# Performance work log

Measured on AMD Instinct MI355X. Metric: run time of the kernel, lower is better.

Reference implementation:

```python
import jax, jax.numpy as jnp
import numpy as np

D_MODEL = 1024
N_HEADS = 16
HEAD_DIM = D_MODEL // N_HEADS
SEQ_LEN = 2048
BATCH = 2
THETA = 10000.0


def _rope_tables(dim, seq_len, theta=THETA):
    freqs = 1.0 / theta ** (jnp.arange(0, dim, 2, dtype=jnp.float32) / dim)  # (dim/2,)
    t = jnp.arange(seq_len, dtype=jnp.float32)
    ang = jnp.outer(t, freqs)  # (S, dim/2)
    # interleave each freq twice to match the (-x_odd, x_even) rotation layout
    cos = jnp.repeat(jnp.cos(ang), 2, axis=-1)  # (S, dim)
    sin = jnp.repeat(jnp.sin(ang), 2, axis=-1)
    return cos, sin


def _apply_rope(x, cos, sin):
    # x: (B, S, H, D); cos/sin: (S, D)
    x_rot = jnp.stack([-x[..., 1::2], x[..., ::2]], axis=-1).reshape(x.shape)
    return x * cos[None, :, None, :] + x_rot * sin[None, :, None, :]


def setup_inputs() -> dict:
    key = jax.random.key(0)
    ks = jax.random.split(key, 9)
    s = 1.0 / np.sqrt(D_MODEL)
    return {
        "x": jax.random.normal(ks[0], (BATCH, SEQ_LEN, D_MODEL), dtype=jnp.float32),
        "wq": jax.random.normal(ks[1], (D_MODEL, D_MODEL), jnp.float32) * s,
        "bq": jnp.zeros((D_MODEL,), jnp.float32),
        "wk": jax.random.normal(ks[2], (D_MODEL, D_MODEL), jnp.float32) * s,
        "bk": jnp.zeros((D_MODEL,), jnp.float32),
        "wv": jax.random.normal(ks[3], (D_MODEL, D_MODEL), jnp.float32) * s,
        "bv": jnp.zeros((D_MODEL,), jnp.float32),
        "wo": jax.random.normal(ks[4], (D_MODEL, D_MODEL), jnp.float32) * s,
        "bo": jnp.zeros((D_MODEL,), jnp.float32),
    }


def reference(x, wq, bq, wk, bk, wv, bv, wo, bo):
    B, S, _ = x.shape
    cos, sin = _rope_tables(HEAD_DIM, S)
    # projections (torch Linear: x @ W^T + b)
    q = (x @ wq.T + bq).reshape(B, S, N_HEADS, HEAD_DIM)
    k = (x @ wk.T + bk).reshape(B, S, N_HEADS, HEAD_DIM)
    v = (x @ wv.T + bv).reshape(B, S, N_HEADS, HEAD_DIM)
    q = _apply_rope(q, cos, sin)
    k = _apply_rope(k, cos, sin)
    # attention: bhqd, bhkd -> bhqk
    scale = 1.0 / np.sqrt(HEAD_DIM)
    scores = jnp.einsum("bqhd,bkhd->bhqk", q, k) * scale
    attn = jax.nn.softmax(scores, axis=-1)
    out = jnp.einsum("bhqk,bkhd->bqhd", attn, v).reshape(B, S, D_MODEL)
    return out @ wo.T + bo
```

## Files before the change

### kernel.cpp

```cpp
#include <hip/hip_runtime.h>

typedef __attribute__((ext_vector_type(8))) __bf16 bf16x8;
typedef __attribute__((ext_vector_type(4))) __bf16 bf16x4;
typedef __attribute__((ext_vector_type(4))) float f32x4;
typedef __attribute__((ext_vector_type(4))) unsigned short ushort4v;

__device__ __forceinline__ unsigned short f2bf(float f) {
  unsigned u = __builtin_bit_cast(unsigned, f);
  u += 0x7fffu + ((u >> 16) & 1u);
  return (unsigned short)(u >> 16);
}

__device__ __forceinline__ void gload16(const void* g, void* l) {
  __builtin_amdgcn_global_load_lds(
      (const __attribute__((address_space(1))) void*)g,
      (__attribute__((address_space(3))) void*)l, 16, 0, 0);
}

__global__ __launch_bounds__(256) void convert_k(
    const float* __restrict__ x, const float* __restrict__ wq,
    const float* __restrict__ wk, const float* __restrict__ wv,
    const float* __restrict__ wo,
    unsigned short* __restrict__ xb, unsigned short* __restrict__ wqkv,
    unsigned short* __restrict__ wob, float* cosT, float* sinT) {
  if (blockIdx.x >= 8192) {
    const int idx = (blockIdx.x - 8192) * 256 + threadIdx.x;
    const int s = idx >> 5, j = idx & 31;
    const float freq = powf(10000.f, -(float)(2 * j) * (1.f / 64.f));
    const float ang = (float)s * freq;
    cosT[idx] = cosf(ang);
    sinT[idx] = sinf(ang);
    return;
  }
  const size_t i = ((size_t)blockIdx.x * 256 + threadIdx.x) * 4;
  const float* src; unsigned short* dst; size_t off;
  if (i < 4194304)      { src = x;  dst = xb;              off = i; }
  else if (i < 5242880) { src = wq; dst = wqkv;            off = i - 4194304; }
  else if (i < 6291456) { src = wk; dst = wqkv + 1048576;  off = i - 5242880; }
  else if (i < 7340032) { src = wv; dst = wqkv + 2097152;  off = i - 6291456; }
  else                  { src = wo; dst = wob;             off = i - 7340032; }
  f32x4 v = *(const f32x4*)(src + off);
  ushort4v o;
  o[0] = f2bf(v[0]); o[1] = f2bf(v[1]); o[2] = f2bf(v[2]); o[3] = f2bf(v[3]);
  *(ushort4v*)(dst + off) = o;
}

template <int EPI>
__global__ __launch_bounds__(256) void gemm_bt_k(
    const unsigned short* __restrict__ A, const unsigned short* __restrict__ B,
    int M, int N, int K,
    unsigned short* __restrict__ Qr, unsigned short* __restrict__ Kr,
    unsigned short* __restrict__ Vt,
    const float* __restrict__ bq, const float* __restrict__ bk,
    const float* __restrict__ bvv,
    const float* __restrict__ cosT, const float* __restrict__ sinT,
    float* __restrict__ Cout, const float* __restrict__ bias) {
  __shared__ char smem[32768];
  const int t = threadIdx.x;
  const int wave = t >> 6, lane = t & 63;
  const int l15 = lane & 15, g = lane >> 4;
  const int nt = N >> 7;
  const int mb = (blockIdx.x / nt) << 7;
  const int nb = (blockIdx.x % nt) << 7;
  const int wm = (wave >> 1) << 6;
  const int wn = (wave & 1) << 6;

  const f32x4 zv = {0.f, 0.f, 0.f, 0.f};
  f32x4 acc[4][4];
#pragma unroll
  for (int i = 0; i < 4; i++)
#pragma unroll
    for (int j = 0; j < 4; j++) acc[i][j] = zv;

  for (int kt = 0; kt < K; kt += 64) {
#pragma unroll
    for (int i = 0; i < 4; i++) {
      const int lin = t * 16 + i * 4096;
      const int r = lin >> 7;
      const int cb = (lin & 127) ^ ((r & 7) << 4);
      gload16((const char*)A + ((size_t)(mb + r) * K + kt) * 2 + cb,
              smem + i * 4096 + wave * 1024);
      gload16((const char*)B + ((size_t)(nb + r) * K + kt) * 2 + cb,
              smem + 16384 + i * 4096 + wave * 1024);
    }
    __syncthreads();

    bf16x8 af[4][2], bfr[4][2];
    const int sw = (l15 & 7) << 4;
#pragma unroll
    for (int mf = 0; mf < 4; mf++) {
      const int r = wm + mf * 16 + l15;
      const int r2 = wn + mf * 16 + l15;
#pragma unroll
      for (int kf = 0; kf < 2; kf++) {
        af[mf][kf]  = *(const bf16x8*)(smem + r * 128 + ((kf * 64 + g * 16) ^ sw));
        bfr[mf][kf] = *(const bf16x8*)(smem + 16384 + r2 * 128 + ((kf * 64 + g * 16) ^ sw));
      }
    }
#pragma unroll
    for (int mf = 0; mf < 4; mf++)
#pragma unroll
      for (int nf = 0; nf < 4; nf++) {
        acc[mf][nf] = __builtin_amdgcn_mfma_f32_16x16x32_bf16(af[mf][0], bfr[nf][0], acc[mf][nf], 0, 0, 0);
        acc[mf][nf] = __builtin_amdgcn_mfma_f32_16x16x32_bf16(af[mf][1], bfr[nf][1], acc[mf][nf], 0, 0, 0);
      }
    __syncthreads();
  }

#pragma unroll
  for (int mf = 0; mf < 4; mf++) {
#pragma unroll
    for (int nf = 0; nf < 4; nf++) {
      const int row0 = mb + wm + mf * 16 + g * 4;
      const int col = nb + wn + nf * 16 + l15;
      if (EPI == 1) {
        const float bsv = bias[col];
#pragma unroll
        for (int r = 0; r < 4; r++)
          Cout[(size_t)(row0 + r) * N + col] = acc[mf][nf][r] + bsv;
      } else {
        const int region = col >> 10;
        const int cc = col & 1023;
        const int h = cc >> 6, d = cc & 63;
        const float bias_v = (region == 0 ? bq : (region == 1 ? bk : bvv))[cc];
        if (region < 2) {
          unsigned short* Ob = (region == 0 ? Qr : Kr);
          const float scl = (region == 0) ? 0.180336880111120425f : 1.0f;
#pragma unroll
          for (int r = 0; r < 4; r++) {
            const int row = row0 + r;
            const int s = row & 2047;
            const int b = row >> 11;
            const float v = acc[mf][nf][r] + bias_v;
            const float p = __shfl_xor(v, 1);
            const float c = cosT[s * 32 + (d >> 1)];
            const float sn = sinT[s * 32 + (d >> 1)];
            float o = (d & 1) ? (v * c + p * sn) : (v * c - p * sn);
            o *= scl;
            Ob[((size_t)(b * 16 + h) * 2048 + s) * 64 + d] = f2bf(o);
          }
        } else {
          ushort4v w;
#pragma unroll
          for (int r = 0; r < 4; r++) w[r] = f2bf(acc[mf][nf][r] + bias_v);
          const int s = row0 & 2047;
          const int b = row0 >> 11;
          *(ushort4v*)(Vt + ((size_t)(b * 16 + h) * 64 + d) * 2048 + s) = w;
        }
      }
    }
  }
}

__global__ __launch_bounds__(256, 4) void flash_k(
    const unsigned short* __restrict__ Qr, const unsigned short* __restrict__ Kr,
    const unsigned short* __restrict__ Vt, unsigned short* __restrict__ Oa) {
  __shared__ char smem[40960];
  const int bid = blockIdx.x;
  const int bh = ((bid & 7) << 2) | ((bid >> 3) & 3);
  const int qt = bid >> 5;
  const int t = threadIdx.x;
  const int wave = t >> 6, lane = t & 63;
  const int l15 = lane & 15, g = lane >> 4;
  char* pbuf = smem + 32768 + wave * 2048;
  const int q0 = qt * 64 + wave * 16;
  const unsigned short* Qb = Qr + ((size_t)bh * 2048 + q0) * 64;
  const char* Kb = (const char*)(Kr + (size_t)bh * 2048 * 64);
  const char* Vb = (const char*)(Vt + (size_t)bh * 64 * 2048);

  const bf16x8 qf0 = *(const bf16x8*)(Qb + l15 * 64 + g * 8);
  const bf16x8 qf1 = *(const bf16x8*)(Qb + l15 * 64 + g * 8 + 32);

  const f32x4 zv = {0.f, 0.f, 0.f, 0.f};
  f32x4 ot[4];
#pragma unroll
  for (int i = 0; i < 4; i++) ot[i] = zv;
  float m = -1e30f, lsum = 0.f;
  const int sw = (l15 & 7) << 4;

#pragma unroll
  for (int i = 0; i < 2; i++) {
    const int lin = t * 16 + i * 4096;
    const int r = lin >> 7;
    const int cb = (lin & 127) ^ ((r & 7) << 4);
    gload16(Kb + (size_t)r * 128 + cb, smem + i * 4096 + wave * 1024);
    gload16(Vb + (size_t)r * 4096 + cb, smem + 8192 + i * 4096 + wave * 1024);
  }
  __syncthreads();

  for (int it = 0; it < 32; ++it) {
    const int cur = it & 1;
    const char* kb = smem + cur * 16384;
    const char* vb = kb + 8192;
    if (it < 31) {
      const int kvn = (it + 1) << 6;
      char* kd = smem + (cur ^ 1) * 16384;
#pragma unroll
      for (int i = 0; i < 2; i++) {
        const int lin = t * 16 + i * 4096;
        const int r = lin >> 7;
        const int cb = (lin & 127) ^ ((r & 7) << 4);
        gload16(Kb + (size_t)(kvn + r) * 128 + cb, kd + i * 4096 + wave * 1024);
        gload16(Vb + (size_t)r * 4096 + kvn * 2 + cb, kd + 8192 + i * 4096 + wave * 1024);
      }
    }
    f32x4 st[4];
#pragma unroll
    for (int s = 0; s < 4; s++) {
      const int rb = (s * 16 + l15) * 128;
      const bf16x8 k0 = *(const bf16x8*)(kb + rb + ((g * 16) ^ sw));
      const bf16x8 k1 = *(const bf16x8*)(kb + rb + ((64 + g * 16) ^ sw));
      f32x4 a = __builtin_amdgcn_mfma_f32_16x16x32_bf16(k0, qf0, zv, 0, 0, 0);
      st[s] = __builtin_amdgcn_mfma_f32_16x16x32_bf16(k1, qf1, a, 0, 0, 0);
    }
    float tmax = st[0][0];
#pragma unroll
    for (int s = 0; s < 4; s++)
#pragma unroll
      for (int e = 0; e < 4; e++) tmax = fmaxf(tmax, st[s][e]);
    tmax = fmaxf(tmax, __shfl_xor(tmax, 16));
    tmax = fmaxf(tmax, __shfl_xor(tmax, 32));
    if (!__all(tmax <= m + 8.0f)) {
      const float mn = fmaxf(m, tmax);
      const float al = __builtin_amdgcn_exp2f(m - mn);
      lsum *= al;
#pragma unroll
      for (int i = 0; i < 4; i++) {
        ot[i][0] *= al; ot[i][1] *= al; ot[i][2] *= al; ot[i][3] *= al;
      }
      m = mn;
    }
    float ls[4];
#pragma unroll
    for (int s = 0; s < 4; s++) {
      ls[s] = 0.f;
#pragma unroll
      for (int e = 0; e < 4; e++) {
        const float p = __builtin_amdgcn_exp2f(st[s][e] - m);
        st[s][e] = p;
        ls[s] += p;
      }
    }
    lsum += (ls[0] + ls[1]) + (ls[2] + ls[3]);
#pragma unroll
    for (int s = 0; s < 4; s++) {
      bf16x4 w;
#pragma unroll
      for (int e = 0; e < 4; e++) w[e] = (__bf16)st[s][e];
      *(bf16x4*)(pbuf + ((l15 * 128 + s * 32 + g * 8) ^ sw)) = w;
    }
    asm volatile("" ::: "memory");
#pragma unroll
    for (int h = 0; h < 2; h++) {
      const bf16x8 pb = *(const bf16x8*)(pbuf + ((l15 * 128 + h * 64 + g * 16) ^ sw));
#pragma unroll
      for (int dc = 0; dc < 4; dc++) {
        const bf16x8 va = *(const bf16x8*)(vb + (dc * 16 + l15) * 128 + ((h * 64 + g * 16) ^ sw));
        ot[dc] = __builtin_amdgcn_mfma_f32_16x16x32_bf16(va, pb, ot[dc], 0, 0, 0);
      }
    }
    __syncthreads();
  }
  lsum += __shfl_xor(lsum, 16);
  lsum += __shfl_xor(lsum, 32);
  const float inv = 1.f / lsum;
  const int b = bh >> 4, h = bh & 15;
  const size_t rowbase = ((size_t)(b * 2048 + q0 + l15)) * 1024 + h * 64;
#pragma unroll
  for (int dc = 0; dc < 4; dc++) {
    bf16x4 w;
#pragma unroll
    for (int r = 0; r < 4; r++) w[r] = (__bf16)(ot[dc][r] * inv);
    *(bf16x4*)(Oa + rowbase + dc * 16 + g * 4) = w;
  }
}

extern "C" void kernel_launch(void* const* d_in, const int* in_sizes, int n_in,
                              void* d_out, int out_size, void* d_ws, size_t ws_size,
                              hipStream_t stream) {
  const float* x  = (const float*)d_in[0];
  const float* wq = (const float*)d_in[1];
  const float* bq = (const float*)d_in[2];
  const float* wk = (const float*)d_in[3];
  const float* bk = (const float*)d_in[4];
  const float* wv = (const float*)d_in[5];
  const float* bv = (const float*)d_in[6];
  const float* wo = (const float*)d_in[7];
  const float* bo = (const float*)d_in[8];
  float* out = (float*)d_out;
  char* ws = (char*)d_ws;

  unsigned short* xb   = (unsigned short*)(ws);
  unsigned short* wqkv = (unsigned short*)(ws + 8388608);
  unsigned short* wob  = (unsigned short*)(ws + 14680064);
  float* cosT          = (float*)(ws + 16777216);
  float* sinT          = (float*)(ws + 17039360);
  unsigned short* Qr   = (unsigned short*)(ws + 17301504);
  unsigned short* Kr   = (unsigned short*)(ws + 25690112);
  unsigned short* Vt   = (unsigned short*)(ws + 34078720);
  unsigned short* Oa   = (unsigned short*)(ws + 42467328);

  convert_k<<<dim3(8448), dim3(256), 0, stream>>>(x, wq, wk, wv, wo, xb, wqkv, wob, cosT, sinT);
  gemm_bt_k<0><<<dim3(32 * 24), dim3(256), 0, stream>>>(
      xb, wqkv, 4096, 3072, 1024, Qr, Kr, Vt, bq, bk, bv, cosT, sinT,
      (float*)nullptr, (const float*)nullptr);
  flash_k<<<dim3(1024), dim3(256), 0, stream>>>(Qr, Kr, Vt, Oa);
  gemm_bt_k<1><<<dim3(32 * 8), dim3(256), 0, stream>>>(
      Oa, wob, 4096, 1024, 1024,
      (unsigned short*)nullptr, (unsigned short*)nullptr, (unsigned short*)nullptr,
      (const float*)nullptr, (const float*)nullptr, (const float*)nullptr,
      cosT, sinT, out, bo);
}
```

Baseline: 136.8 us.

## Switch flash attention to 32x32x16 MFMA with register-resident P via permlane swap

Rewrites the attention kernel so each of two waves handles 32 query rows using 32x32x16 bf16 MFMA instead of four waves on 16x16x32 tiles. The P matrix is packed to bf16 with v_cvt_pk_bf16_f32 and rearranged between lane halves with v_permlane32_swap. This removes the per-wave LDS round trip for P and shrinks shared memory. Each block now has 128 threads, which cuts per-block parallelism and gives each wave more accumulator registers and more KV loads to issue.

```diff
diff --git a/kernel.cpp b/kernel.cpp
--- a/kernel.cpp
+++ b/kernel.cpp
@@ -3,12 +3,24 @@
 typedef __attribute__((ext_vector_type(8))) __bf16 bf16x8;
 typedef __attribute__((ext_vector_type(4))) __bf16 bf16x4;
 typedef __attribute__((ext_vector_type(4))) float f32x4;
+typedef __attribute__((ext_vector_type(16))) float f32x16;
+typedef __attribute__((ext_vector_type(4))) int i32x4;
 typedef __attribute__((ext_vector_type(4))) unsigned short ushort4v;
 
 __device__ __forceinline__ unsigned short f2bf(float f) {
   unsigned u = __builtin_bit_cast(unsigned, f);
   u += 0x7fffu + ((u >> 16) & 1u);
   return (unsigned short)(u >> 16);
+}
+
+__device__ __forceinline__ unsigned cvt_pk_bf16(float lo, float hi) {
+  unsigned r;
+  asm("v_cvt_pk_bf16_f32 %0, %1, %2" : "=v"(r) : "v"(lo), "v"(hi));
+  return r;
+}
+
+__device__ __forceinline__ void pl32swap(unsigned& a, unsigned& b) {
+  asm("v_permlane32_swap_b32 %0, %1" : "+v"(a), "+v"(b));
 }
 
 __device__ __forceinline__ void gload16(const void* g, void* l) {
@@ -152,126 +164,127 @@
   }
 }
 
-__global__ __launch_bounds__(256, 4) void flash_k(
+__global__ __launch_bounds__(128, 4) void flash_k(
     const unsigned short* __restrict__ Qr, const unsigned short* __restrict__ Kr,
     const unsigned short* __restrict__ Vt, unsigned short* __restrict__ Oa) {
-  __shared__ char smem[40960];
+  __shared__ char smem[32768];
   const int bid = blockIdx.x;
   const int bh = ((bid & 7) << 2) | ((bid >> 3) & 3);
   const int qt = bid >> 5;
   const int t = threadIdx.x;
   const int wave = t >> 6, lane = t & 63;
-  const int l15 = lane & 15, g = lane >> 4;
-  char* pbuf = smem + 32768 + wave * 2048;
-  const int q0 = qt * 64 + wave * 16;
+  const int l31 = lane & 31, h32 = lane >> 5;
+  const int q0 = qt * 64 + wave * 32;
   const unsigned short* Qb = Qr + ((size_t)bh * 2048 + q0) * 64;
   const char* Kb = (const char*)(Kr + (size_t)bh * 2048 * 64);
   const char* Vb = (const char*)(Vt + (size_t)bh * 64 * 2048);
 
-  const bf16x8 qf0 = *(const bf16x8*)(Qb + l15 * 64 + g * 8);
-  const bf16x8 qf1 = *(const bf16x8*)(Qb + l15 * 64 + g * 8 + 32);
-
-  const f32x4 zv = {0.f, 0.f, 0.f, 0.f};
-  f32x4 ot[4];
-#pragma unroll
-  for (int i = 0; i < 4; i++) ot[i] = zv;
+  bf16x8 qB[4];
+#pragma unroll
+  for (int t4 = 0; t4 < 4; t4++)
+    qB[t4] = *(const bf16x8*)(Qb + l31 * 64 + t4 * 16 + h32 * 8);
+
+  f32x16 ot0 = {0,0,0,0,0,0,0,0,0,0,0,0,0,0,0,0};
+  f32x16 ot1 = {0,0,0,0,0,0,0,0,0,0,0,0,0,0,0,0};
   float m = -1e30f, lsum = 0.f;
-  const int sw = (l15 & 7) << 4;
-
-#pragma unroll
-  for (int i = 0; i < 2; i++) {
-    const int lin = t * 16 + i * 4096;
-    const int r = lin >> 7;
-    const int cb = (lin & 127) ^ ((r & 7) << 4);
-    gload16(Kb + (size_t)r * 128 + cb, smem + i * 4096 + wave * 1024);
-    gload16(Vb + (size_t)r * 4096 + cb, smem + 8192 + i * 4096 + wave * 1024);
+  const int swv = (l31 & 7) << 4;
+
+  const int sr0 = t >> 3;
+  const int sc0 = (t & 7) * 16;
+#pragma unroll
+  for (int i = 0; i < 4; i++) {
+    const int r = sr0 + i * 16;
+    const int cb = sc0 ^ ((r & 7) << 4);
+    gload16(Kb + (size_t)r * 128 + cb, smem + i * 2048 + wave * 1024);
+    gload16(Vb + (size_t)r * 4096 + cb, smem + 8192 + i * 2048 + wave * 1024);
   }
   __syncthreads();
 
   for (int it = 0; it < 32; ++it) {
-    const int cur = it & 1;
-    const char* kb = smem + cur * 16384;
-    const char* vb = kb + 8192;
+    const char* kb = smem + (it & 1) * 16384;
+    const char* vbuf = kb + 8192;
     if (it < 31) {
       const int kvn = (it + 1) << 6;
-      char* kd = smem + (cur ^ 1) * 16384;
-#pragma unroll
-      for (int i = 0; i < 2; i++) {
-        const int lin = t * 16 + i * 4096;
-        const int r = lin >> 7;
-        const int cb = (lin & 127) ^ ((r & 7) << 4);
-        gload16(Kb + (size_t)(kvn + r) * 128 + cb, kd + i * 4096 + wave * 1024);
-        gload16(Vb + (size_t)r * 4096 + kvn * 2 + cb, kd + 8192 + i * 4096 + wave * 1024);
-      }
-    }
-    f32x4 st[4];
-#pragma unroll
-    for (int s = 0; s < 4; s++) {
-      const int rb = (s * 16 + l15) * 128;
-      const bf16x8 k0 = *(const bf16x8*)(kb + rb + ((g * 16) ^ sw));
-      const bf16x8 k1 = *(const bf16x8*)(kb + rb + ((64 + g * 16) ^ sw));
-      f32x4 a = __builtin_amdgcn_mfma_f32_16x16x32_bf16(k0, qf0, zv, 0, 0, 0);
-      st[s] = __builtin_amdgcn_mfma_f32_16x16x32_bf16(k1, qf1, a, 0, 0, 0);
-    }
-    float tmax = st[0][0];
-#pragma unroll
-    for (int s = 0; s < 4; s++)
-#pragma unroll
-      for (int e = 0; e < 4; e++) tmax = fmaxf(tmax, st[s][e]);
-    tmax = fmaxf(tmax, __shfl_xor(tmax, 16));
+      char* kd = smem + ((it & 1) ^ 1) * 16384;
+#pragma unroll
+      for (int i = 0; i < 4; i++) {
+        const int r = sr0 + i * 16;
+        const int cb = sc0 ^ ((r & 7) << 4);
+        gload16(Kb + (size_t)(kvn + r) * 128 + cb, kd + i * 2048 + wave * 1024);
+        gload16(Vb + (size_t)r * 4096 + kvn * 2 + cb, kd + 8192 + i * 2048 + wave * 1024);
+      }
+    }
+    f32x16 st0 = {0,0,0,0,0,0,0,0,0,0,0,0,0,0,0,0};
+    f32x16 st1 = {0,0,0,0,0,0,0,0,0,0,0,0,0,0,0,0};
+#pragma unroll
+    for (int t4 = 0; t4 < 4; t4++) {
+      const int r0 = l31, r1 = 32 + l31;
+      const bf16x8 ka0 = *(const bf16x8*)(kb + r0 * 128 + ((t4 * 32 + h32 * 16) ^ swv));
+      const bf16x8 ka1 = *(const bf16x8*)(kb + r1 * 128 + ((t4 * 32 + h32 * 16) ^ swv));
+      st0 = __builtin_amdgcn_mfma_f32_32x32x16_bf16(ka0, qB[t4], st0, 0, 0, 0);
+      st1 = __builtin_amdgcn_mfma_f32_32x32x16_bf16(ka1, qB[t4], st1, 0, 0, 0);
+    }
+    float tmax = st0[0];
+#pragma unroll
+    for (int e = 1; e < 16; e++) tmax = fmaxf(tmax, st0[e]);
+#pragma unroll
+    for (int e = 0; e < 16; e++) tmax = fmaxf(tmax, st1[e]);
     tmax = fmaxf(tmax, __shfl_xor(tmax, 32));
     if (!__all(tmax <= m + 8.0f)) {
       const float mn = fmaxf(m, tmax);
       const float al = __builtin_amdgcn_exp2f(m - mn);
       lsum *= al;
 #pragma unroll
-      for (int i = 0; i < 4; i++) {
-        ot[i][0] *= al; ot[i][1] *= al; ot[i][2] *= al; ot[i][3] *= al;
-      }
+      for (int e = 0; e < 16; e++) { ot0[e] *= al; ot1[e] *= al; }
       m = mn;
     }
-    float ls[4];
-#pragma unroll
-    for (int s = 0; s < 4; s++) {
-      ls[s] = 0.f;
-#pragma unroll
-      for (int e = 0; e < 4; e++) {
-        const float p = __builtin_amdgcn_exp2f(st[s][e] - m);
-        st[s][e] = p;
-        ls[s] += p;
-      }
-    }
-    lsum += (ls[0] + ls[1]) + (ls[2] + ls[3]);
-#pragma unroll
-    for (int s = 0; s < 4; s++) {
-      bf16x4 w;
-#pragma unroll
-      for (int e = 0; e < 4; e++) w[e] = (__bf16)st[s][e];
-      *(bf16x4*)(pbuf + ((l15 * 128 + s * 32 + g * 8) ^ sw)) = w;
-    }
-    asm volatile("" ::: "memory");
-#pragma unroll
-    for (int h = 0; h < 2; h++) {
-      const bf16x8 pb = *(const bf16x8*)(pbuf + ((l15 * 128 + h * 64 + g * 16) ^ sw));
-#pragma unroll
-      for (int dc = 0; dc < 4; dc++) {
-        const bf16x8 va = *(const bf16x8*)(vb + (dc * 16 + l15) * 128 + ((h * 64 + g * 16) ^ sw));
-        ot[dc] = __builtin_amdgcn_mfma_f32_16x16x32_bf16(va, pb, ot[dc], 0, 0, 0);
+    float ls0 = 0.f, ls1 = 0.f;
+#pragma unroll
+    for (int e = 0; e < 16; e++) {
+      const float p0 = __builtin_amdgcn_exp2f(st0[e] - m);
+      const float p1 = __builtin_amdgcn_exp2f(st1[e] - m);
+      st0[e] = p0; st1[e] = p1;
+      ls0 += p0; ls1 += p1;
+    }
+    lsum += ls0 + ls1;
+#pragma unroll
+    for (int tile = 0; tile < 2; tile++) {
+      unsigned p2[8];
+#pragma unroll
+      for (int c = 0; c < 8; c++)
+        p2[c] = tile ? cvt_pk_bf16(st1[2 * c], st1[2 * c + 1])
+                     : cvt_pk_bf16(st0[2 * c], st0[2 * c + 1]);
+#pragma unroll
+      for (int sg = 0; sg < 2; sg++) {
+        unsigned b0 = p2[sg * 4 + 0], b2 = p2[sg * 4 + 2];
+        unsigned b1 = p2[sg * 4 + 1], b3 = p2[sg * 4 + 3];
+        pl32swap(b0, b2);
+        pl32swap(b1, b3);
+        const i32x4 bw = {(int)b0, (int)b1, (int)b2, (int)b3};
+        const bf16x8 pb = __builtin_bit_cast(bf16x8, bw);
+        const int kvbyte = tile * 64 + sg * 32 + h32 * 16;
+        const bf16x8 va0 = *(const bf16x8*)(vbuf + l31 * 128 + (kvbyte ^ swv));
+        const bf16x8 va1 = *(const bf16x8*)(vbuf + (32 + l31) * 128 + (kvbyte ^ swv));
+        ot0 = __builtin_amdgcn_mfma_f32_32x32x16_bf16(va0, pb, ot0, 0, 0, 0);
+        ot1 = __builtin_amdgcn_mfma_f32_32x32x16_bf16(va1, pb, ot1, 0, 0, 0);
       }
     }
     __syncthreads();
   }
-  lsum += __shfl_xor(lsum, 16);
   lsum += __shfl_xor(lsum, 32);
   const float inv = 1.f / lsum;
-  const int b = bh >> 4, h = bh & 15;
-  const size_t rowbase = ((size_t)(b * 2048 + q0 + l15)) * 1024 + h * 64;
-#pragma unroll
-  for (int dc = 0; dc < 4; dc++) {
-    bf16x4 w;
-#pragma unroll
-    for (int r = 0; r < 4; r++) w[r] = (__bf16)(ot[dc][r] * inv);
-    *(bf16x4*)(Oa + rowbase + dc * 16 + g * 4) = w;
+  const int b = bh >> 4, hh = bh & 15;
+  const size_t rowbase = ((size_t)(b * 2048 + q0 + l31)) * 1024 + hh * 64;
+#pragma unroll
+  for (int dt = 0; dt < 2; dt++) {
+#pragma unroll
+    for (int grp = 0; grp < 4; grp++) {
+      bf16x4 w;
+#pragma unroll
+      for (int e = 0; e < 4; e++)
+        w[e] = (__bf16)((dt ? ot1[grp * 4 + e] : ot0[grp * 4 + e]) * inv);
+      *(bf16x4*)(Oa + rowbase + dt * 32 + grp * 8 + 4 * h32) = w;
+    }
   }
 }
 
@@ -304,7 +317,7 @@
   gemm_bt_k<0><<<dim3(32 * 24), dim3(256), 0, stream>>>(
       xb, wqkv, 4096, 3072, 1024, Qr, Kr, Vt, bq, bk, bv, cosT, sinT,
       (float*)nullptr, (const float*)nullptr);
-  flash_k<<<dim3(1024), dim3(256), 0, stream>>>(Qr, Kr, Vt, Oa);
+  flash_k<<<dim3(1024), dim3(128), 0, stream>>>(Qr, Kr, Vt, Oa);
   gemm_bt_k<1><<<dim3(32 * 8), dim3(256), 0, stream>>>(
       Oa, wob, 4096, 1024, 1024,
       (unsigned short*)nullptr, (unsigned short*)nullptr, (unsigned short*)nullptr,
```

Result: no change. 138.0 us (+0.9%).
